# Performance work log

Hardware: AMD Instinct MI355X
Metric: run time of the kernel (lower is better)

## Reference

```python
import jax, jax.numpy as jnp
import numpy as np

S, L, E, H, V, T, A = 4096, 16, 512, 512, 100000, 64, 50


def setup_inputs() -> dict:
    key = jax.random.key(0)
    ks = jax.random.split(key, 20)
    f32 = jnp.float32
    n = lambda k, shape: jax.random.normal(k, shape, f32) * 0.05
    return {
        "sent_in": jax.random.randint(ks[0], (S,), 0, V),
        "char_in": jax.random.randint(ks[1], (S, L), 0, A),
        "lengths": jax.random.randint(ks[2], (S,), 1, L + 1),
        "word_emb": n(ks[3], (V, E)),
        "char_emb": n(ks[4], (A, E)),
        "Wih_w": n(ks[5], (4 * H, E)),
        "Whh_w": n(ks[6], (4 * H, H)),
        "bih_w": n(ks[7], (4 * H,)),
        "bhh_w": n(ks[8], (4 * H,)),
        "Wih_c": n(ks[9], (4 * H, E)),
        "Whh_c": n(ks[10], (4 * H, H)),
        "bih_c": n(ks[11], (4 * H,)),
        "bhh_c": n(ks[12], (4 * H,)),
        "Ww2t": n(ks[13], (T, H)),
        "bw2t": n(ks[14], (T,)),
        "Wc2t": n(ks[15], (T, H)),
        "bc2t": n(ks[16], (T,)),
    }


def _lstm(xs, mask, W_ih, W_hh, b_ih, b_hh):
    """xs: [T, B, E], mask: [T, B] (1 = valid). Returns hs: [T, B, H].
    PyTorch gate order i, f, g, o. Carry is frozen on masked steps."""
    Hd = W_hh.shape[1]
    B = xs.shape[1]
    gx = jnp.einsum('tbe,ge->tbg', xs, W_ih) + b_ih  # precompute input gates

    def step(carry, inp):
        h, c = carry
        g, m = inp
        gates = g + h @ W_hh.T + b_hh
        i, f, gg, o = jnp.split(gates, 4, axis=-1)
        c_new = jax.nn.sigmoid(f) * c + jax.nn.sigmoid(i) * jnp.tanh(gg)
        h_new = jax.nn.sigmoid(o) * jnp.tanh(c_new)
        mm = m[:, None]
        h_new = jnp.where(mm, h_new, h)
        c_new = jnp.where(mm, c_new, c)
        return (h_new, c_new), h_new

    h0 = jnp.zeros((B, Hd), xs.dtype)
    c0 = jnp.zeros((B, Hd), xs.dtype)
    _, hs = jax.lax.scan(step, (h0, c0), (gx, mask))
    return hs


def reference(sent_in, char_in, lengths, word_emb, char_emb,
              Wih_w, Whh_w, bih_w, bhh_w,
              Wih_c, Whh_c, bih_c, bhh_c,
              Ww2t, bw2t, Wc2t, bc2t):
    # word-level LSTM over the sentence (batch = 1)
    xs_w = word_emb[sent_in][:, None, :]                  # [S, 1, E]
    mask_w = jnp.ones((sent_in.shape[0], 1), jnp.bool_)
    hs_w = _lstm(xs_w, mask_w, Wih_w, Whh_w, bih_w, bhh_w)  # [S, 1, H]
    word_scores = hs_w[:, 0, :] @ Ww2t.T + bw2t           # [S, T]

    # char-level LSTM: all words processed as one batch, masked by length
    xs_c = char_emb[char_in].transpose(1, 0, 2)           # [L, S, E]
    Lm = char_in.shape[1]
    mask_c = jnp.arange(Lm)[:, None] < lengths[None, :]   # [L, S]
    hs_c = _lstm(xs_c, mask_c, Wih_c, Whh_c, bih_c, bhh_c)  # [L, S, H]
    out_sum = jnp.sum(hs_c * mask_c[:, :, None].astype(hs_c.dtype), axis=0)  # [S, H]
    char_scores = out_sum @ Wc2t.T + bc2t                 # [S, T]

    return jax.nn.log_softmax(char_scores + word_scores, axis=1)
```

## Files before the change

kernel.cpp:

```cpp
#include <hip/hip_runtime.h>
#include <cstdint>
#include <cstddef>

#define S_  4096
#define L_  16
#define E_  512
#define H_  512
#define G4_ 2048
#define T_  64
#define WORD_WGS 32

__device__ __forceinline__ float sigmoidf_(float x) {
    return 1.0f / (1.0f + __expf(-x));
}
__device__ __forceinline__ float fast_tanhf_(float x) {
    return 1.0f - 2.0f / (__expf(2.0f * x) + 1.0f);
}

#define BM 128
#define BN 128
#define BK 16

__global__ __launch_bounds__(256, 2)
void gemm_nt_kernel(const float* __restrict__ A1, const int* __restrict__ idxA,
                    int idxStride, int idxOff, const float* __restrict__ A2,
                    const float* __restrict__ B1, const float* __restrict__ B2,
                    int Ksplit, int K, int N, float* __restrict__ C)
{
    __shared__ float As[BK][BM + 4];
    __shared__ float Bs[BK][BN + 4];
    __shared__ int   rIdx[BM];

    const int tid = threadIdx.x;
    const int m0 = blockIdx.y * BM;
    const int n0 = blockIdx.x * BN;
    if (idxA && tid < BM)
        rIdx[tid] = idxA[(size_t)(m0 + tid) * idxStride + idxOff];

    const int tx = tid & 15;
    const int ty = tid >> 4;
    const int ar = tid >> 2;
    const int aq = tid & 3;

    float acc[8][8];
#pragma unroll
    for (int i = 0; i < 8; ++i)
#pragma unroll
        for (int j = 0; j < 8; ++j) acc[i][j] = 0.f;

    for (int k0 = 0; k0 < K; k0 += BK) {
        __syncthreads();
        const bool firstHalf = (k0 < Ksplit);
        const int  kk0 = firstHalf ? k0 : (k0 - Ksplit);
#pragma unroll
        for (int part = 0; part < 2; ++part) {
            const int row = ar + part * 64;
            float4 av, bv;
            if (firstHalf) {
                const int grA = idxA ? rIdx[row] : (m0 + row);
                av = *(const float4*)(A1 + (size_t)grA * Ksplit + kk0 + aq * 4);
                bv = *(const float4*)(B1 + (size_t)(n0 + row) * Ksplit + kk0 + aq * 4);
            } else {
                const int Kr = K - Ksplit;
                av = *(const float4*)(A2 + (size_t)(m0 + row) * Kr + kk0 + aq * 4);
                bv = *(const float4*)(B2 + (size_t)(n0 + row) * Kr + kk0 + aq * 4);
            }
            As[aq * 4 + 0][row] = av.x; As[aq * 4 + 1][row] = av.y;
            As[aq * 4 + 2][row] = av.z; As[aq * 4 + 3][row] = av.w;
            Bs[aq * 4 + 0][row] = bv.x; Bs[aq * 4 + 1][row] = bv.y;
            Bs[aq * 4 + 2][row] = bv.z; Bs[aq * 4 + 3][row] = bv.w;
        }
        __syncthreads();
#pragma unroll
        for (int kk = 0; kk < BK; ++kk) {
            const float4 a0 = *(const float4*)&As[kk][ty * 4];
            const float4 a1 = *(const float4*)&As[kk][64 + ty * 4];
            const float4 b0 = *(const float4*)&Bs[kk][tx * 4];
            const float4 b1 = *(const float4*)&Bs[kk][64 + tx * 4];
            const float a[8] = {a0.x, a0.y, a0.z, a0.w, a1.x, a1.y, a1.z, a1.w};
            const float b[8] = {b0.x, b0.y, b0.z, b0.w, b1.x, b1.y, b1.z, b1.w};
#pragma unroll
            for (int i = 0; i < 8; ++i)
#pragma unroll
                for (int j = 0; j < 8; ++j)
                    acc[i][j] = fmaf(a[i], b[j], acc[i][j]);
        }
    }
#pragma unroll
    for (int ri = 0; ri < 2; ++ri)
#pragma unroll
        for (int i = 0; i < 4; ++i) {
            const int m = m0 + ri * 64 + ty * 4 + i;
            float4 v0 = make_float4(acc[ri * 4 + i][0], acc[ri * 4 + i][1],
                                    acc[ri * 4 + i][2], acc[ri * 4 + i][3]);
            float4 v1 = make_float4(acc[ri * 4 + i][4], acc[ri * 4 + i][5],
                                    acc[ri * 4 + i][6], acc[ri * 4 + i][7]);
            *(float4*)(C + (size_t)m * N + n0 + tx * 4)      = v0;
            *(float4*)(C + (size_t)m * N + n0 + 64 + tx * 4) = v1;
        }
}

__global__ __launch_bounds__(512)
void word_lstm_kernel(const float* __restrict__ gxw, const float* __restrict__ Whh,
                      const float* __restrict__ bih, const float* __restrict__ bhh,
                      float* __restrict__ hsw, float* __restrict__ h_buf,
                      unsigned int* __restrict__ cnt, int T)
{
    const int wg   = blockIdx.x;
    const int base = wg * 16;
    const int tid  = threadIdx.x;
    const int r    = tid >> 3;
    const int p    = tid & 7;
    const int grow = (r >> 4) * 512 + base + (r & 15);

    float4 w[16];
    const float4* Wrow = (const float4*)(Whh + (size_t)grow * 512);
#pragma unroll
    for (int kk = 0; kk < 16; ++kk) w[kk] = Wrow[kk * 8 + p];

    __shared__ float h_lds[512];
    __shared__ float gate_lds[64];
    __shared__ float bsum[64];
    if (tid < 64) {
        const int gr = (tid >> 4) * 512 + base + (tid & 15);
        bsum[tid] = bih[gr] + bhh[gr];
    }
    if (tid < 128) ((float4*)h_lds)[tid] = make_float4(0.f, 0.f, 0.f, 0.f);
    float cstate = 0.f;
    __syncthreads();

    for (int t = 0; t < T; ++t) {
        float gxv = 0.f;
        if (p == 0) gxv = gxw[(size_t)t * G4_ + grow];

        float s = 0.f;
#pragma unroll
        for (int kk = 0; kk < 16; ++kk) {
            const float4 h4 = ((const float4*)h_lds)[kk * 8 + p];
            s = fmaf(w[kk].x, h4.x, s);
            s = fmaf(w[kk].y, h4.y, s);
            s = fmaf(w[kk].z, h4.z, s);
            s = fmaf(w[kk].w, h4.w, s);
        }
        s += __shfl_xor(s, 1);
        s += __shfl_xor(s, 2);
        s += __shfl_xor(s, 4);
        if (p == 0) gate_lds[r] = s + gxv + bsum[r];
        __syncthreads();

        if (tid < 16) {
            const float gi = gate_lds[tid];
            const float gf = gate_lds[16 + tid];
            const float gg = gate_lds[32 + tid];
            const float go = gate_lds[48 + tid];
            const float cn = sigmoidf_(gf) * cstate + sigmoidf_(gi) * fast_tanhf_(gg);
            cstate = cn;
            const float hn = sigmoidf_(go) * fast_tanhf_(cn);
            hsw[(size_t)t * H_ + base + tid] = hn;
            __hip_atomic_store(&h_buf[((t + 1) & 1) * H_ + base + tid], hn,
                               __ATOMIC_RELAXED, __HIP_MEMORY_SCOPE_AGENT);
        }
        __syncthreads();

        if (tid == 0) {
            __hip_atomic_fetch_add(&cnt[t], 1u, __ATOMIC_RELEASE, __HIP_MEMORY_SCOPE_AGENT);
            while (__hip_atomic_load(&cnt[t], __ATOMIC_ACQUIRE, __HIP_MEMORY_SCOPE_AGENT)
                   < (unsigned)WORD_WGS)
                __builtin_amdgcn_s_sleep(2);
        }
        __syncthreads();

        {
            const float* src = h_buf + ((t + 1) & 1) * H_;
            h_lds[tid] = __hip_atomic_load(&src[tid], __ATOMIC_RELAXED,
                                           __HIP_MEMORY_SCOPE_AGENT);
        }
        __syncthreads();
    }
}

__global__ __launch_bounds__(256)
void char_update_kernel(const float* __restrict__ gates,
                        const float* __restrict__ bih, const float* __restrict__ bhh,
                        const int* __restrict__ lengths, int l,
                        float* __restrict__ h, float* __restrict__ c,
                        float* __restrict__ osum)
{
    const int gid = blockIdx.x * blockDim.x + threadIdx.x;
    const int s  = gid >> 7;
    const int j4 = (gid & 127) * 4;
    const bool valid = (l < lengths[s]);

    const float4 gi = *(const float4*)(gates + (size_t)s * G4_ + j4);
    const float4 gf = *(const float4*)(gates + (size_t)s * G4_ + 512 + j4);
    const float4 gg = *(const float4*)(gates + (size_t)s * G4_ + 1024 + j4);
    const float4 go = *(const float4*)(gates + (size_t)s * G4_ + 1536 + j4);
    const float4 bi0 = *(const float4*)(bih + j4);
    const float4 bi1 = *(const float4*)(bih + 512 + j4);
    const float4 bi2 = *(const float4*)(bih + 1024 + j4);
    const float4 bi3 = *(const float4*)(bih + 1536 + j4);
    const float4 bh0 = *(const float4*)(bhh + j4);
    const float4 bh1 = *(const float4*)(bhh + 512 + j4);
    const float4 bh2 = *(const float4*)(bhh + 1024 + j4);
    const float4 bh3 = *(const float4*)(bhh + 1536 + j4);

    float4 hv = *(float4*)(h + (size_t)s * H_ + j4);
    float4 cv = *(float4*)(c + (size_t)s * H_ + j4);
    float4 ov = *(float4*)(osum + (size_t)s * H_ + j4);

#define UPD(X)                                                                  \
    {                                                                           \
        const float I = sigmoidf_(gi.X + bi0.X + bh0.X);                        \
        const float F = sigmoidf_(gf.X + bi1.X + bh1.X);                        \
        const float G = fast_tanhf_(gg.X + bi2.X + bh2.X);                      \
        const float O = sigmoidf_(go.X + bi3.X + bh3.X);                        \
        const float cn = F * cv.X + I * G;                                      \
        const float hn = O * fast_tanhf_(cn);                                   \
        if (valid) { cv.X = cn; hv.X = hn; ov.X += hn; }                        \
    }
    UPD(x) UPD(y) UPD(z) UPD(w)
#undef UPD

    *(float4*)(h + (size_t)s * H_ + j4)    = hv;
    *(float4*)(c + (size_t)s * H_ + j4)    = cv;
    *(float4*)(osum + (size_t)s * H_ + j4) = ov;
}

__global__ __launch_bounds__(64)
void scores_kernel(const float* __restrict__ hsw, const float* __restrict__ osum,
                   const float* __restrict__ Ww2t, const float* __restrict__ bw2t,
                   const float* __restrict__ Wc2t, const float* __restrict__ bc2t,
                   float* __restrict__ out)
{
    const int s = blockIdx.x;
    const int t = threadIdx.x;
    __shared__ float4 hrow[128], orow[128];
    hrow[t]      = ((const float4*)(hsw + (size_t)s * H_))[t];
    hrow[t + 64] = ((const float4*)(hsw + (size_t)s * H_))[t + 64];
    orow[t]      = ((const float4*)(osum + (size_t)s * H_))[t];
    orow[t + 64] = ((const float4*)(osum + (size_t)s * H_))[t + 64];
    __syncthreads();

    float acc = bw2t[t] + bc2t[t];
    const float4* w1 = (const float4*)(Ww2t + (size_t)t * H_);
    const float4* w2 = (const float4*)(Wc2t + (size_t)t * H_);
#pragma unroll 8
    for (int k = 0; k < 128; ++k) {
        const float4 a = w1[k], hb = hrow[k];
        acc = fmaf(a.x, hb.x, acc); acc = fmaf(a.y, hb.y, acc);
        acc = fmaf(a.z, hb.z, acc); acc = fmaf(a.w, hb.w, acc);
        const float4 b = w2[k], ob = orow[k];
        acc = fmaf(b.x, ob.x, acc); acc = fmaf(b.y, ob.y, acc);
        acc = fmaf(b.z, ob.z, acc); acc = fmaf(b.w, ob.w, acc);
    }
    float m = acc;
#pragma unroll
    for (int off = 32; off > 0; off >>= 1) m = fmaxf(m, __shfl_xor(m, off));
    float sum = __expf(acc - m);
#pragma unroll
    for (int off = 32; off > 0; off >>= 1) sum += __shfl_xor(sum, off);
    out[(size_t)s * T_ + t] = acc - m - __logf(sum);
}

extern "C" void kernel_launch(void* const* d_in, const int* in_sizes, int n_in,
                              void* d_out, int out_size, void* d_ws, size_t ws_size,
                              hipStream_t stream)
{
    (void)in_sizes; (void)n_in; (void)out_size; (void)ws_size;

    const int*   sent_in  = (const int*)d_in[0];
    const int*   char_in  = (const int*)d_in[1];
    const int*   lengths  = (const int*)d_in[2];
    const float* word_emb = (const float*)d_in[3];
    const float* char_emb = (const float*)d_in[4];
    const float* Wih_w    = (const float*)d_in[5];
    const float* Whh_w    = (const float*)d_in[6];
    const float* bih_w    = (const float*)d_in[7];
    const float* bhh_w    = (const float*)d_in[8];
    const float* Wih_c    = (const float*)d_in[9];
    const float* Whh_c    = (const float*)d_in[10];
    const float* bih_c    = (const float*)d_in[11];
    const float* bhh_c    = (const float*)d_in[12];
    const float* Ww2t     = (const float*)d_in[13];
    const float* bw2t     = (const float*)d_in[14];
    const float* Wc2t     = (const float*)d_in[15];
    const float* bc2t     = (const float*)d_in[16];

    char* ws = (char*)d_ws;
    float* gxw  = (float*)(ws + 0);
    float* hsw  = (float*)(ws + 33554432);
    float* h_c  = (float*)(ws + 41943040);
    float* c_c  = (float*)(ws + 50331648);
    float* osum = (float*)(ws + 58720256);
    float* hbuf = (float*)(ws + 67108864);
    unsigned int* cnt = (unsigned int*)(ws + 67112960);

    hipMemsetAsync(hbuf, 0, 4096, stream);
    hipMemsetAsync(cnt,  0, 16384, stream);
    hipMemsetAsync(h_c,  0, 8388608, stream);
    hipMemsetAsync(c_c,  0, 8388608, stream);
    hipMemsetAsync(osum, 0, 8388608, stream);

    const dim3 gemmGrid(G4_ / BN, S_ / BM);

    gemm_nt_kernel<<<gemmGrid, 256, 0, stream>>>(
        word_emb, sent_in, 1, 0, nullptr,
        Wih_w, nullptr, E_, E_, G4_, gxw);

    word_lstm_kernel<<<WORD_WGS, 512, 0, stream>>>(
        gxw, Whh_w, bih_w, bhh_w, hsw, hbuf, cnt, S_);

    for (int l = 0; l < L_; ++l) {
        gemm_nt_kernel<<<gemmGrid, 256, 0, stream>>>(
            char_emb, char_in, L_, l, h_c,
            Wih_c, Whh_c, E_, E_ + H_, G4_, gxw );
        char_update_kernel<<<(S_ * 128) / 256, 256, 0, stream>>>(
            gxw, bih_c, bhh_c, lengths, l, h_c, c_c, osum);
    }

    scores_kernel<<<S_, 64, 0, stream>>>(hsw, osum, Ww2t, bw2t, Wc2t, bc2t,
                                         (float*)d_out);
}
```

Baseline: 16.05 ms.

## Fuse word and char LSTMs into one persistent kernel running concurrently

Replaces the separate word-LSTM kernel and the 16 char GEMM/update launch pairs with a single persistent kernel. The first 32 workgroups run the sequential word recurrence while 256 further workgroups run the char LSTM, fusing the gate GEMM with the cell update and using grid-wide atomic barriers between steps. This is meant to hide the char work behind the long serial word recurrence and to cut launch overhead and the round trip of the gate tensor through memory. The word path also prefetches the next step's input gates and keeps weights pinned in registers. It depends on all 288 workgroups being co-resident, otherwise the spin barriers deadlock, and the char workgroups may contend with the latency-critical word workgroups.

```diff
diff --git a/kernel.cpp b/kernel.cpp
--- a/kernel.cpp
+++ b/kernel.cpp
@@ -9,6 +9,8 @@
 #define G4_ 2048
 #define T_  64
 #define WORD_WGS 32
+#define CHAR_WGS 256
+#define ALL_WGS  (WORD_WGS + CHAR_WGS)
 
 __device__ __forceinline__ float sigmoidf_(float x) {
     return 1.0f / (1.0f + __expf(-x));
@@ -27,15 +29,15 @@
                     const float* __restrict__ B1, const float* __restrict__ B2,
                     int Ksplit, int K, int N, float* __restrict__ C)
 {
-    __shared__ float As[BK][BM + 4];
-    __shared__ float Bs[BK][BN + 4];
-    __shared__ int   rIdx[BM];
+    __shared__ float As_[BK][BM + 4];
+    __shared__ float Bs_[BK][BN + 4];
+    __shared__ int   rIdx_[BM];
 
     const int tid = threadIdx.x;
     const int m0 = blockIdx.y * BM;
     const int n0 = blockIdx.x * BN;
     if (idxA && tid < BM)
-        rIdx[tid] = idxA[(size_t)(m0 + tid) * idxStride + idxOff];
+        rIdx_[tid] = idxA[(size_t)(m0 + tid) * idxStride + idxOff];
 
     const int tx = tid & 15;
     const int ty = tid >> 4;
@@ -57,7 +59,7 @@
             const int row = ar + part * 64;
             float4 av, bv;
             if (firstHalf) {
-                const int grA = idxA ? rIdx[row] : (m0 + row);
+                const int grA = idxA ? rIdx_[row] : (m0 + row);
                 av = *(const float4*)(A1 + (size_t)grA * Ksplit + kk0 + aq * 4);
                 bv = *(const float4*)(B1 + (size_t)(n0 + row) * Ksplit + kk0 + aq * 4);
             } else {
@@ -65,18 +67,18 @@
                 av = *(const float4*)(A2 + (size_t)(m0 + row) * Kr + kk0 + aq * 4);
                 bv = *(const float4*)(B2 + (size_t)(n0 + row) * Kr + kk0 + aq * 4);
             }
-            As[aq * 4 + 0][row] = av.x; As[aq * 4 + 1][row] = av.y;
-            As[aq * 4 + 2][row] = av.z; As[aq * 4 + 3][row] = av.w;
-            Bs[aq * 4 + 0][row] = bv.x; Bs[aq * 4 + 1][row] = bv.y;
-            Bs[aq * 4 + 2][row] = bv.z; Bs[aq * 4 + 3][row] = bv.w;
+            As_[aq * 4 + 0][row] = av.x; As_[aq * 4 + 1][row] = av.y;
+            As_[aq * 4 + 2][row] = av.z; As_[aq * 4 + 3][row] = av.w;
+            Bs_[aq * 4 + 0][row] = bv.x; Bs_[aq * 4 + 1][row] = bv.y;
+            Bs_[aq * 4 + 2][row] = bv.z; Bs_[aq * 4 + 3][row] = bv.w;
         }
         __syncthreads();
 #pragma unroll
         for (int kk = 0; kk < BK; ++kk) {
-            const float4 a0 = *(const float4*)&As[kk][ty * 4];
-            const float4 a1 = *(const float4*)&As[kk][64 + ty * 4];
-            const float4 b0 = *(const float4*)&Bs[kk][tx * 4];
-            const float4 b1 = *(const float4*)&Bs[kk][64 + tx * 4];
+            const float4 a0 = *(const float4*)&As_[kk][ty * 4];
+            const float4 a1 = *(const float4*)&As_[kk][64 + ty * 4];
+            const float4 b0 = *(const float4*)&Bs_[kk][tx * 4];
+            const float4 b1 = *(const float4*)&Bs_[kk][64 + tx * 4];
             const float a[8] = {a0.x, a0.y, a0.z, a0.w, a1.x, a1.y, a1.z, a1.w};
             const float b[8] = {b0.x, b0.y, b0.z, b0.w, b1.x, b1.y, b1.z, b1.w};
 #pragma unroll
@@ -100,130 +102,233 @@
         }
 }
 
-__global__ __launch_bounds__(512)
-void word_lstm_kernel(const float* __restrict__ gxw, const float* __restrict__ Whh,
-                      const float* __restrict__ bih, const float* __restrict__ bhh,
-                      float* __restrict__ hsw, float* __restrict__ h_buf,
-                      unsigned int* __restrict__ cnt, int T)
+__global__ __launch_bounds__(512, 4)
+void fused_lstm_kernel(const float* __restrict__ gxw,
+                       const float* __restrict__ Whh_w,
+                       const float* __restrict__ bih_w,
+                       const float* __restrict__ bhh_w,
+                       float* __restrict__ hsw, float* __restrict__ h_buf,
+                       unsigned int* __restrict__ cnt,
+                       const int* __restrict__ char_in,
+                       const int* __restrict__ lengths,
+                       const float* __restrict__ char_emb,
+                       const float* __restrict__ Wih_c,
+                       const float* __restrict__ Whh_c,
+                       const float* __restrict__ bih_c,
+                       const float* __restrict__ bhh_c,
+                       float* __restrict__ h_c, float* __restrict__ c_c,
+                       float* __restrict__ osum)
 {
-    const int wg   = blockIdx.x;
-    const int base = wg * 16;
-    const int tid  = threadIdx.x;
-    const int r    = tid >> 3;
-    const int p    = tid & 7;
-    const int grow = (r >> 4) * 512 + base + (r & 15);
-
-    float4 w[16];
-    const float4* Wrow = (const float4*)(Whh + (size_t)grow * 512);
-#pragma unroll
-    for (int kk = 0; kk < 16; ++kk) w[kk] = Wrow[kk * 8 + p];
-
     __shared__ float h_lds[512];
     __shared__ float gate_lds[64];
-    __shared__ float bsum[64];
-    if (tid < 64) {
-        const int gr = (tid >> 4) * 512 + base + (tid & 15);
-        bsum[tid] = bih[gr] + bhh[gr];
+    __shared__ float wb[64];
+    __shared__ float As[16][132];
+    __shared__ float Bs[16][260];
+    __shared__ int   rIdx[128];
+    __shared__ int   lens[128];
+    __shared__ float cb[256];
+
+    const int tid = threadIdx.x;
+
+    if (blockIdx.x < WORD_WGS) {
+        const int wg   = blockIdx.x;
+        const int base = wg * 16;
+        const int r    = tid >> 3;
+        const int p    = tid & 7;
+        const int grow = (r >> 4) * 512 + base + (r & 15);
+
+        float wreg[64];
+        {
+            const float4* Wrow = (const float4*)(Whh_w + (size_t)grow * 512);
+#pragma unroll
+            for (int kk = 0; kk < 16; ++kk) {
+                const float4 v = Wrow[kk * 8 + p];
+                wreg[kk * 4 + 0] = v.x; wreg[kk * 4 + 1] = v.y;
+                wreg[kk * 4 + 2] = v.z; wreg[kk * 4 + 3] = v.w;
+            }
+#pragma unroll
+            for (int i = 0; i < 64; ++i) asm volatile("" : "+v"(wreg[i]));
+        }
+        if (tid < 64) {
+            const int gr = (tid >> 4) * 512 + base + (tid & 15);
+            wb[tid] = bih_w[gr] + bhh_w[gr];
+        }
+        if (tid < 128) ((float4*)h_lds)[tid] = make_float4(0.f, 0.f, 0.f, 0.f);
+        float cstate = 0.f;
+        __syncthreads();
+
+        float gxv = (p == 0) ? gxw[grow] : 0.f;
+        for (int t = 0; t < S_; ++t) {
+            float gxn = 0.f;
+            if (p == 0 && t + 1 < S_) gxn = gxw[(size_t)(t + 1) * G4_ + grow];
+
+            float s = 0.f;
+#pragma unroll
+            for (int kk = 0; kk < 16; ++kk) {
+                const float4 h4 = ((const float4*)h_lds)[kk * 8 + p];
+                s = fmaf(wreg[kk * 4 + 0], h4.x, s);
+                s = fmaf(wreg[kk * 4 + 1], h4.y, s);
+                s = fmaf(wreg[kk * 4 + 2], h4.z, s);
+                s = fmaf(wreg[kk * 4 + 3], h4.w, s);
+            }
+            s += __shfl_xor(s, 1);
+            s += __shfl_xor(s, 2);
+            s += __shfl_xor(s, 4);
+            if (p == 0) gate_lds[r] = s + gxv + wb[r];
+            __syncthreads();
+
+            if (tid < 16) {
+                const float gi = gate_lds[tid];
+                const float gf = gate_lds[16 + tid];
+                const float gg = gate_lds[32 + tid];
+                const float go = gate_lds[48 + tid];
+                const float cn = sigmoidf_(gf) * cstate + sigmoidf_(gi) * fast_tanhf_(gg);
+                cstate = cn;
+                const float hn = sigmoidf_(go) * fast_tanhf_(cn);
+                hsw[(size_t)t * H_ + base + tid] = hn;
+                __hip_atomic_store(&h_buf[((t + 1) & 1) * H_ + base + tid], hn,
+                                   __ATOMIC_RELAXED, __HIP_MEMORY_SCOPE_AGENT);
+            }
+            __syncthreads();
+
+            if (tid == 0) {
+                __hip_atomic_fetch_add(&cnt[0], 1u, __ATOMIC_RELEASE,
+                                       __HIP_MEMORY_SCOPE_AGENT);
+                while (__hip_atomic_load(&cnt[0], __ATOMIC_ACQUIRE,
+                                         __HIP_MEMORY_SCOPE_AGENT)
+                       < (unsigned)WORD_WGS * (unsigned)(t + 1))
+                    __builtin_amdgcn_s_sleep(2);
+            }
+            __syncthreads();
+
+            h_lds[tid] = __hip_atomic_load(&h_buf[((t + 1) & 1) * H_ + tid],
+                                           __ATOMIC_RELAXED, __HIP_MEMORY_SCOPE_AGENT);
+            __syncthreads();
+            gxv = gxn;
+        }
+    } else {
+        const int cw  = blockIdx.x - WORD_WGS;
+        const int m0  = (cw >> 3) * 128;
+        const int hu0 = (cw & 7) * 64;
+        const int tx  = tid & 31;
+        const int ty  = tid >> 5;
+
+        if (tid < 128) lens[tid] = lengths[m0 + tid];
+        if (tid < 256) {
+            const int g = tid >> 6, ul = tid & 63;
+            const int br = g * 512 + hu0 + ul;
+            cb[tid] = bih_c[br] + bhh_c[br];
+        }
+
+        for (int l = 0; l < L_; ++l) {
+            if (tid < 128) rIdx[tid] = char_in[(size_t)(m0 + tid) * L_ + l];
+
+            float acc[8][8];
+#pragma unroll
+            for (int i = 0; i < 8; ++i)
+#pragma unroll
+                for (int j = 0; j < 8; ++j) acc[i][j] = 0.f;
+
+            for (int kt = 0; kt < 64; ++kt) {
+                const int k0 = kt * 16;
+                __syncthreads();
+                const int row = tid >> 2, q = tid & 3;
+                float4 av;
+                if (k0 < 512) {
+                    av = *(const float4*)(char_emb + (size_t)rIdx[row] * E_ + k0 + q * 4);
+                } else {
+                    const float* hp = h_c + (size_t)(m0 + row) * H_ + (k0 - 512) + q * 4;
+                    av.x = __hip_atomic_load(hp + 0, __ATOMIC_RELAXED, __HIP_MEMORY_SCOPE_AGENT);
+                    av.y = __hip_atomic_load(hp + 1, __ATOMIC_RELAXED, __HIP_MEMORY_SCOPE_AGENT);
+                    av.z = __hip_atomic_load(hp + 2, __ATOMIC_RELAXED, __HIP_MEMORY_SCOPE_AGENT);
+                    av.w = __hip_atomic_load(hp + 3, __ATOMIC_RELAXED, __HIP_MEMORY_SCOPE_AGENT);
+                }
+                As[q * 4 + 0][row] = av.x; As[q * 4 + 1][row] = av.y;
+                As[q * 4 + 2][row] = av.z; As[q * 4 + 3][row] = av.w;
+#pragma unroll
+                for (int cc = 0; cc < 2; ++cc) {
+                    const int c  = row + cc * 128;
+                    const int g  = c >> 6, u = c & 63;
+                    const int br = g * 512 + hu0 + u;
+                    const float* bp = (k0 < 512)
+                        ? (Wih_c + (size_t)br * E_ + k0 + q * 4)
+                        : (Whh_c + (size_t)br * H_ + (k0 - 512) + q * 4);
+                    const float4 bv = *(const float4*)bp;
+                    Bs[q * 4 + 0][c] = bv.x; Bs[q * 4 + 1][c] = bv.y;
+                    Bs[q * 4 + 2][c] = bv.z; Bs[q * 4 + 3][c] = bv.w;
+                }
+                __syncthreads();
+#pragma unroll
+                for (int kk = 0; kk < 16; ++kk) {
+                    const float4 a0 = *(const float4*)&As[kk][ty * 8];
+                    const float4 a1 = *(const float4*)&As[kk][ty * 8 + 4];
+                    const float a[8] = {a0.x, a0.y, a0.z, a0.w, a1.x, a1.y, a1.z, a1.w};
+                    float b[8];
+#pragma unroll
+                    for (int g = 0; g < 4; ++g) {
+                        const float2 bg = *(const float2*)&Bs[kk][g * 64 + 2 * tx];
+                        b[(g << 1)]     = bg.x;
+                        b[(g << 1) | 1] = bg.y;
+                    }
+#pragma unroll
+                    for (int i = 0; i < 8; ++i)
+#pragma unroll
+                        for (int j = 0; j < 8; ++j)
+                            acc[i][j] = fmaf(a[i], b[j], acc[i][j]);
+                }
+            }
+
+            __syncthreads();
+            if (tid == 0) {
+                __hip_atomic_fetch_add(&cnt[32], 1u, __ATOMIC_RELEASE,
+                                       __HIP_MEMORY_SCOPE_AGENT);
+                while (__hip_atomic_load(&cnt[32], __ATOMIC_ACQUIRE,
+                                         __HIP_MEMORY_SCOPE_AGENT)
+                       < (unsigned)CHAR_WGS * (unsigned)(2 * l + 1))
+                    __builtin_amdgcn_s_sleep(2);
+            }
+            __syncthreads();
+
+#pragma unroll
+            for (int i = 0; i < 8; ++i) {
+                const int mr = ty * 8 + i;
+                const int m  = m0 + mr;
+                if (l < lens[mr]) {
+                    const int hl = 2 * tx;
+                    float* cp = c_c  + (size_t)m * H_ + hu0 + hl;
+                    float* op = osum + (size_t)m * H_ + hu0 + hl;
+                    float2 c2 = *(float2*)cp;
+                    float2 o2 = *(float2*)op;
+#pragma unroll
+                    for (int u = 0; u < 2; ++u) {
+                        const float I = sigmoidf_(acc[i][0 + u] + cb[      hl + u]);
+                        const float F = sigmoidf_(acc[i][2 + u] + cb[ 64 + hl + u]);
+                        const float G = fast_tanhf_(acc[i][4 + u] + cb[128 + hl + u]);
+                        const float O = sigmoidf_(acc[i][6 + u] + cb[192 + hl + u]);
+                        const float cv = u ? c2.y : c2.x;
+                        const float cn = F * cv + I * G;
+                        const float hn = O * fast_tanhf_(cn);
+                        if (u) { c2.y = cn; o2.y += hn; } else { c2.x = cn; o2.x += hn; }
+                        __hip_atomic_store(h_c + (size_t)m * H_ + hu0 + hl + u, hn,
+                                           __ATOMIC_RELAXED, __HIP_MEMORY_SCOPE_AGENT);
+                    }
+                    *(float2*)cp = c2;
+                    *(float2*)op = o2;
+                }
+            }
+
+            __syncthreads();
+            if (tid == 0) {
+                __hip_atomic_fetch_add(&cnt[32], 1u, __ATOMIC_RELEASE,
+                                       __HIP_MEMORY_SCOPE_AGENT);
+                while (__hip_atomic_load(&cnt[32], __ATOMIC_ACQUIRE,
+                                         __HIP_MEMORY_SCOPE_AGENT)
+                       < (unsigned)CHAR_WGS * (unsigned)(2 * l + 2))
+                    __builtin_amdgcn_s_sleep(2);
+            }
+            __syncthreads();
+        }
     }
-    if (tid < 128) ((float4*)h_lds)[tid] = make_float4(0.f, 0.f, 0.f, 0.f);
-    float cstate = 0.f;
-    __syncthreads();
-
-    for (int t = 0; t < T; ++t) {
-        float gxv = 0.f;
-        if (p == 0) gxv = gxw[(size_t)t * G4_ + grow];
-
-        float s = 0.f;
-#pragma unroll
-        for (int kk = 0; kk < 16; ++kk) {
-            const float4 h4 = ((const float4*)h_lds)[kk * 8 + p];
-            s = fmaf(w[kk].x, h4.x, s);
-            s = fmaf(w[kk].y, h4.y, s);
-            s = fmaf(w[kk].z, h4.z, s);
-            s = fmaf(w[kk].w, h4.w, s);
-        }
-        s += __shfl_xor(s, 1);
-        s += __shfl_xor(s, 2);
-        s += __shfl_xor(s, 4);
-        if (p == 0) gate_lds[r] = s + gxv + bsum[r];
-        __syncthreads();
-
-        if (tid < 16) {
-            const float gi = gate_lds[tid];
-            const float gf = gate_lds[16 + tid];
-            const float gg = gate_lds[32 + tid];
-            const float go = gate_lds[48 + tid];
-            const float cn = sigmoidf_(gf) * cstate + sigmoidf_(gi) * fast_tanhf_(gg);
-            cstate = cn;
-            const float hn = sigmoidf_(go) * fast_tanhf_(cn);
-            hsw[(size_t)t * H_ + base + tid] = hn;
-            __hip_atomic_store(&h_buf[((t + 1) & 1) * H_ + base + tid], hn,
-                               __ATOMIC_RELAXED, __HIP_MEMORY_SCOPE_AGENT);
-        }
-        __syncthreads();
-
-        if (tid == 0) {
-            __hip_atomic_fetch_add(&cnt[t], 1u, __ATOMIC_RELEASE, __HIP_MEMORY_SCOPE_AGENT);
-            while (__hip_atomic_load(&cnt[t], __ATOMIC_ACQUIRE, __HIP_MEMORY_SCOPE_AGENT)
-                   < (unsigned)WORD_WGS)
-                __builtin_amdgcn_s_sleep(2);
-        }
-        __syncthreads();
-
-        {
-            const float* src = h_buf + ((t + 1) & 1) * H_;
-            h_lds[tid] = __hip_atomic_load(&src[tid], __ATOMIC_RELAXED,
-                                           __HIP_MEMORY_SCOPE_AGENT);
-        }
-        __syncthreads();
-    }
-}
-
-__global__ __launch_bounds__(256)
-void char_update_kernel(const float* __restrict__ gates,
-                        const float* __restrict__ bih, const float* __restrict__ bhh,
-                        const int* __restrict__ lengths, int l,
-                        float* __restrict__ h, float* __restrict__ c,
-                        float* __restrict__ osum)
-{
-    const int gid = blockIdx.x * blockDim.x + threadIdx.x;
-    const int s  = gid >> 7;
-    const int j4 = (gid & 127) * 4;
-    const bool valid = (l < lengths[s]);
-
-    const float4 gi = *(const float4*)(gates + (size_t)s * G4_ + j4);
-    const float4 gf = *(const float4*)(gates + (size_t)s * G4_ + 512 + j4);
-    const float4 gg = *(const float4*)(gates + (size_t)s * G4_ + 1024 + j4);
-    const float4 go = *(const float4*)(gates + (size_t)s * G4_ + 1536 + j4);
-    const float4 bi0 = *(const float4*)(bih + j4);
-    const float4 bi1 = *(const float4*)(bih + 512 + j4);
-    const float4 bi2 = *(const float4*)(bih + 1024 + j4);
-    const float4 bi3 = *(const float4*)(bih + 1536 + j4);
-    const float4 bh0 = *(const float4*)(bhh + j4);
-    const float4 bh1 = *(const float4*)(bhh + 512 + j4);
-    const float4 bh2 = *(const float4*)(bhh + 1024 + j4);
-    const float4 bh3 = *(const float4*)(bhh + 1536 + j4);
-
-    float4 hv = *(float4*)(h + (size_t)s * H_ + j4);
-    float4 cv = *(float4*)(c + (size_t)s * H_ + j4);
-    float4 ov = *(float4*)(osum + (size_t)s * H_ + j4);
-
-#define UPD(X)                                                                  \
-    {                                                                           \
-        const float I = sigmoidf_(gi.X + bi0.X + bh0.X);                        \
-        const float F = sigmoidf_(gf.X + bi1.X + bh1.X);                        \
-        const float G = fast_tanhf_(gg.X + bi2.X + bh2.X);                      \
-        const float O = sigmoidf_(go.X + bi3.X + bh3.X);                        \
-        const float cn = F * cv.X + I * G;                                      \
-        const float hn = O * fast_tanhf_(cn);                                   \
-        if (valid) { cv.X = cn; hv.X = hn; ov.X += hn; }                        \
-    }
-    UPD(x) UPD(y) UPD(z) UPD(w)
-#undef UPD
-
-    *(float4*)(h + (size_t)s * H_ + j4)    = hv;
-    *(float4*)(c + (size_t)s * H_ + j4)    = cv;
-    *(float4*)(osum + (size_t)s * H_ + j4) = ov;
 }
 
 __global__ __launch_bounds__(64)
@@ -302,21 +407,14 @@
     hipMemsetAsync(osum, 0, 8388608, stream);
 
     const dim3 gemmGrid(G4_ / BN, S_ / BM);
-
     gemm_nt_kernel<<<gemmGrid, 256, 0, stream>>>(
         word_emb, sent_in, 1, 0, nullptr,
         Wih_w, nullptr, E_, E_, G4_, gxw);
 
-    word_lstm_kernel<<<WORD_WGS, 512, 0, stream>>>(
-        gxw, Whh_w, bih_w, bhh_w, hsw, hbuf, cnt, S_);
-
-    for (int l = 0; l < L_; ++l) {
-        gemm_nt_kernel<<<gemmGrid, 256, 0, stream>>>(
-            char_emb, char_in, L_, l, h_c,
-            Wih_c, Whh_c, E_, E_ + H_, G4_, gxw );
-        char_update_kernel<<<(S_ * 128) / 256, 256, 0, stream>>>(
-            gxw, bih_c, bhh_c, lengths, l, h_c, c_c, osum);
-    }
+    fused_lstm_kernel<<<ALL_WGS, 512, 0, stream>>>(
+        gxw, Whh_w, bih_w, bhh_w, hsw, hbuf, cnt,
+        char_in, lengths, char_emb, Wih_c, Whh_c, bih_c, bhh_c,
+        h_c, c_c, osum);
 
     scores_kernel<<<S_, 64, 0, stream>>>(hsw, osum, Ww2t, bw2t, Wc2t, bc2t,
                                          (float*)d_out);
```

New measurement: 14.88 ms. 7.3% less time.
